# Kernel optimization log

Measured on AMD Instinct MI355X. Metric: run time of the kernel, lower is better.

Reference implementation:

```python
import jax, jax.numpy as jnp
import numpy as np

BETA = 1.0
POWER_ITERS = 9
EPS = 1e-12  # F.normalize default eps


def _normalize(v):
    # L2 normalize over dim=1 of [B, N, 1], matching F.normalize(x, dim=1)
    n = jnp.linalg.norm(v, axis=1, keepdims=True)
    return v / jnp.maximum(n, EPS)


def _dominant_eigenvalue(A, x):
    # A: [B, N, N], x: [B, N, 1]
    for _ in range(POWER_ITERS):
        x = _normalize(jnp.matmul(A, x))
    Ax = jnp.matmul(A, x)[..., 0]              # [B, N]
    num = jnp.sum(Ax * x[..., 0], axis=1)      # x^T A x
    den = jnp.sum(x[..., 0] ** 2, axis=1)      # ||x||^2 (== 1 after normalize)
    return num / den, x


def setup_inputs() -> dict:
    key = jax.random.key(0)
    k1, k2 = jax.random.split(key)
    B, C, H, W = 256, 2048, 7, 7
    x = jax.random.normal(k1, (B, C, H, W), dtype=jnp.float32)
    x0 = _normalize(jax.random.normal(k2, (B, H * W, 1), dtype=jnp.float32))
    return {"x": x, "x0": x0}


def reference(x, x0):
    B, C, H, W = x.shape
    N = H * W
    Wm = x.reshape(B, C, N)
    # ATA = W^T W : [B, N, N]
    ATA = jnp.einsum('bcn,bcm->bnm', Wm, Wm)
    # first power iteration: largest eigenvalue; x0 is a no_grad constant
    largest, x1 = _dominant_eigenvalue(ATA, jax.lax.stop_gradient(x0))
    I = jnp.eye(N, dtype=ATA.dtype)
    shifted = ATA - largest[:, None, None] * I
    # second power iteration warm-started from detached x1 (torch stores last_x detached)
    tmp, _ = _dominant_eigenvalue(shifted, jax.lax.stop_gradient(x1))
    smallest = tmp + largest
    penalty = BETA * (largest / smallest - 1.0) ** 2
    return jnp.sum(penalty) / B
```

## Files before the change

### kernel.cpp

```cpp
#include <hip/hip_runtime.h>
#include <hip/hip_bf16.h>
#include <stdint.h>


#define BATCH 256
#define CDIM  2048
#define NDIM  49
#define QK    512
#define NQ    4
#define CHUNK 64
#define NCHUNK (QK / CHUNK)
#define CHUNK_FLOATS (CHUNK * NDIM)
#define CHUNK_F4 (CHUNK_FLOATS / 4)
#define CPAD (CHUNK_FLOATS + 16)
#define PSIZE (NDIM * NDIM)
#define ASTRIDE 53

typedef __bf16 bf16x8 __attribute__((ext_vector_type(8)));
typedef float  f32x16 __attribute__((ext_vector_type(16)));

__device__ inline void async_load16(const float* g, float* l) {
  __builtin_amdgcn_global_load_lds(
      (const __attribute__((address_space(1))) void*)g,
      (__attribute__((address_space(3))) void*)l,
      16 , 0 , 0 );
}

__global__ __launch_bounds__(256, 4) void gram_kernel(
    const float* __restrict__ x, float* __restrict__ partial,
    float* __restrict__ out) {
  __shared__ float raw[2][CPAD];

  const int tid  = threadIdx.x;
  const int bidx = blockIdx.x;
  const int batch = bidx >> 2;
  const int q     = bidx & 3;
  const int lane = tid & 63;
  const int wv   = tid >> 6;
  const int ln   = lane & 31;
  const int hf   = lane >> 5;
  const int qm   = wv >> 1, qn = wv & 1;
  const int m = qm * 32 + ln;
  const int n = qn * 32 + ln;

  if (bidx == 0 && tid == 0) out[0] = 0.f;

  const float* gbase = x + (size_t)batch * (CDIM * NDIM)
                         + (size_t)q * (QK * NDIM);

  f32x16 c1, c2, c3;
#pragma unroll
  for (int i = 0; i < 16; ++i) { c1[i] = 0.f; c2[i] = 0.f; c3[i] = 0.f; }

#pragma unroll
  for (int i = 0; i < (CHUNK_F4 + 255) / 256; ++i) {
    int slot = i * 256 + tid;
    if (slot < CHUNK_F4) async_load16(gbase + slot * 4, &raw[0][slot * 4]);
  }

  for (int ch = 0; ch < NCHUNK; ++ch) {
    __syncthreads();
    const int cur = ch & 1;
    if (ch + 1 < NCHUNK) {
      const float* gch = gbase + (ch + 1) * CHUNK_FLOATS;
      float* dst = raw[cur ^ 1];
#pragma unroll
      for (int i = 0; i < (CHUNK_F4 + 255) / 256; ++i) {
        int slot = i * 256 + tid;
        if (slot < CHUNK_F4) async_load16(gch + slot * 4, &dst[slot * 4]);
      }
    }

    const float* buf = raw[cur];
#pragma unroll
    for (int s = 0; s < CHUNK / 16; ++s) {
      const int kk = s * 16 + hf * 8;
      const float* pa = &buf[kk * NDIM + m];
      const float* pb = &buf[kk * NDIM + n];
      bf16x8 ah, al, bh, bl;
#pragma unroll
      for (int j = 0; j < 8; ++j) {
        float av = pa[j * NDIM];
        __bf16 h = (__bf16)av;
        ah[j] = h;
        al[j] = (__bf16)(av - (float)h);
        float bv = pb[j * NDIM];
        __bf16 hb = (__bf16)bv;
        bh[j] = hb;
        bl[j] = (__bf16)(bv - (float)hb);
      }
      c1 = __builtin_amdgcn_mfma_f32_32x32x16_bf16(ah, bh, c1, 0, 0, 0);
      c2 = __builtin_amdgcn_mfma_f32_32x32x16_bf16(ah, bl, c2, 0, 0, 0);
      c3 = __builtin_amdgcn_mfma_f32_32x32x16_bf16(al, bh, c3, 0, 0, 0);
    }
  }

  float* outp = partial + (size_t)bidx * PSIZE;
#pragma unroll
  for (int r = 0; r < 16; ++r) {
    int row = (r & 3) + 8 * (r >> 2) + 4 * hf;
    int mm = qm * 32 + row;
    if (mm < NDIM && n < NDIM)
      outp[mm * NDIM + n] = c1[r] + c2[r] + c3[r];
  }
}

__global__ __launch_bounds__(64) void eigen_kernel(
    const float* __restrict__ partial, const float* __restrict__ x0,
    float* __restrict__ out) {
  __shared__ float A[NDIM * ASTRIDE];
  __shared__ float xv[64];

  const int b = blockIdx.x;
  const int t = threadIdx.x;
  const float* p0 = partial + (size_t)(NQ * b) * PSIZE;

  for (int idx = t; idx < NDIM * NDIM; idx += 64) {
    int r = idx / NDIM;
    int c = idx - r * NDIM;
    float v = 0.f;
#pragma unroll
    for (int qq = 0; qq < NQ; ++qq) v += p0[qq * PSIZE + idx];
    A[r * ASTRIDE + c] = v;
  }
  if (t < NDIM) xv[t] = x0[b * NDIM + t];
  __syncthreads();

  auto rayleigh_power = [&](float shift) -> float {
    for (int it = 0; it < 9; ++it) {
      float y = 0.f;
      if (t < NDIM) {
        const float* Ar = &A[t * ASTRIDE];
#pragma unroll 7
        for (int k = 0; k < NDIM; ++k) y = fmaf(Ar[k], xv[k], y);
        y -= shift * xv[t];
      }
      float s = y * y;
#pragma unroll
      for (int o = 32; o; o >>= 1) s += __shfl_xor(s, o, 64);
      float nrm = fmaxf(sqrtf(s), 1e-12f);
      __syncthreads();
      if (t < NDIM) xv[t] = y / nrm;
      __syncthreads();
    }
    float yy = 0.f;
    if (t < NDIM) {
      const float* Ar = &A[t * ASTRIDE];
#pragma unroll 7
      for (int k = 0; k < NDIM; ++k) yy = fmaf(Ar[k], xv[k], yy);
      yy -= shift * xv[t];
    }
    float num = (t < NDIM) ? yy * xv[t] : 0.f;
    float den = (t < NDIM) ? xv[t] * xv[t] : 0.f;
#pragma unroll
    for (int o = 32; o; o >>= 1) {
      num += __shfl_xor(num, o, 64);
      den += __shfl_xor(den, o, 64);
    }
    return num / den;
  };

  float largest = rayleigh_power(0.f);
  float tmp = rayleigh_power(largest);
  float smallest = tmp + largest;

  if (t == 0) {
    float r = largest / smallest - 1.f;
    atomicAdd(out, r * r * (1.0f / (float)BATCH));
  }
}

extern "C" void kernel_launch(void* const* d_in, const int* in_sizes, int n_in,
                              void* d_out, int out_size, void* d_ws,
                              size_t ws_size, hipStream_t stream) {
  const float* x  = (const float*)d_in[0];
  const float* x0 = (const float*)d_in[1];
  float* out = (float*)d_out;
  float* partial = (float*)d_ws;

  gram_kernel<<<1024, 256, 0, stream>>>(x, partial, out);
  eigen_kernel<<<BATCH, 64, 0, stream>>>(partial, x0, out);
}
```

Baseline: 177.7 us.

## Fuse Gram and eigen kernels with last-block reduction and symmetric split-bf16 MFMA

Merges the Gram-matrix kernel and the eigenvalue kernel into one launch. The last of the four quarter-blocks per batch, found through an atomic counter, sums the partials and runs the power iterations. The split-bf16 product drops one of three MFMAs by using symmetry: the al*bh term is taken from the transpose of ah*bl, staged through LDS. Loads switch from async global-to-LDS copies of raw fp32 to register prefetch with the bf16 hi/lo conversion done once before storing to LDS. This saves a launch and removes redundant conversions and MFMAs, but adds a memset, atomics and fences, and the eigen phase now runs inside a 256-thread block in which only a few threads do work.

New measurement: 355.9 us. 2x slower.

```diff
diff --git a/kernel.cpp b/kernel.cpp
--- a/kernel.cpp
+++ b/kernel.cpp
@@ -7,130 +7,145 @@
 #define CDIM  2048
 #define NDIM  49
 #define QK    512
-#define NQ    4
 #define CHUNK 64
 #define NCHUNK (QK / CHUNK)
-#define CHUNK_FLOATS (CHUNK * NDIM)
-#define CHUNK_F4 (CHUNK_FLOATS / 4)
-#define CPAD (CHUNK_FLOATS + 16)
+#define KP    72
+#define TILE_ELEMS (64 * KP)
 #define PSIZE (NDIM * NDIM)
-#define ASTRIDE 53
+#define ESTR  65
+#define ASTR  53
+#define CNT_OFF (1024 * PSIZE)
 
 typedef __bf16 bf16x8 __attribute__((ext_vector_type(8)));
 typedef float  f32x16 __attribute__((ext_vector_type(16)));
 
-__device__ inline void async_load16(const float* g, float* l) {
-  __builtin_amdgcn_global_load_lds(
-      (const __attribute__((address_space(1))) void*)g,
-      (__attribute__((address_space(3))) void*)l,
-      16 , 0 , 0 );
-}
-
-__global__ __launch_bounds__(256, 4) void gram_kernel(
-    const float* __restrict__ x, float* __restrict__ partial,
+__global__ __launch_bounds__(256, 4) void ofpenalty_fused(
+    const float* __restrict__ x, const float* __restrict__ x0,
+    float* __restrict__ partial, unsigned int* __restrict__ cnt,
+    float* __restrict__ acc, unsigned int* __restrict__ done,
     float* __restrict__ out) {
-  __shared__ float raw[2][CPAD];
-
-  const int tid  = threadIdx.x;
-  const int bidx = blockIdx.x;
+  __shared__ __align__(16) char smem[4 * TILE_ELEMS * 2];
+  __shared__ int flag;
+  __bf16* tile = (__bf16*)smem;
+  float* Ebuf  = (float*)smem;
+  float* Aeig  = (float*)smem;
+  float* xv    = (float*)(smem + 10400);
+
+  const int tid   = threadIdx.x;
+  const int bidx  = blockIdx.x;
   const int batch = bidx >> 2;
   const int q     = bidx & 3;
-  const int lane = tid & 63;
-  const int wv   = tid >> 6;
-  const int ln   = lane & 31;
-  const int hf   = lane >> 5;
-  const int qm   = wv >> 1, qn = wv & 1;
-  const int m = qm * 32 + ln;
+  const int w     = tid >> 6;
+  const int lane  = tid & 63;
+  const int ln    = lane & 31;
+  const int hf    = lane >> 5;
+  const int qm = w >> 1, qn = w & 1;
+  const int rowA = qm * 32 + ln;
+  const int rowB = qn * 32 + ln;
+
+  const float* gbase = x + ((size_t)batch * CDIM + (size_t)q * QK) * NDIM;
+
+  f32x16 c1, cE;
+#pragma unroll
+  for (int i = 0; i < 16; ++i) { c1[i] = 0.f; cE[i] = 0.f; }
+
+  float L[2][8];
+
+  if (lane < NDIM) {
+#pragma unroll
+    for (int kk = 0; kk < 2; ++kk) {
+      const int kg = w + kk * 4;
+#pragma unroll
+      for (int j = 0; j < 8; ++j)
+        L[kk][j] = gbase[(size_t)(kg * 8 + j) * NDIM + lane];
+    }
+  }
+
+  for (int ch = 0; ch < NCHUNK; ++ch) {
+    const int buf = ch & 1;
+    if (lane < NDIM) {
+#pragma unroll
+      for (int kk = 0; kk < 2; ++kk) {
+        const int kg = w + kk * 4;
+        bf16x8 h8, l8;
+#pragma unroll
+        for (int j = 0; j < 8; ++j) {
+          float v = L[kk][j];
+          __bf16 h = (__bf16)v;
+          h8[j] = h;
+          l8[j] = (__bf16)(v - (float)h);
+        }
+        *(bf16x8*)(tile + (buf * 2 + 0) * TILE_ELEMS + lane * KP + kg * 8) = h8;
+        *(bf16x8*)(tile + (buf * 2 + 1) * TILE_ELEMS + lane * KP + kg * 8) = l8;
+      }
+    }
+    __syncthreads();
+    if (ch + 1 < NCHUNK && lane < NDIM) {
+      const float* cb = gbase + (size_t)((ch + 1) * CHUNK) * NDIM + lane;
+#pragma unroll
+      for (int kk = 0; kk < 2; ++kk) {
+        const int kg = w + kk * 4;
+#pragma unroll
+        for (int j = 0; j < 8; ++j)
+          L[kk][j] = cb[(size_t)(kg * 8 + j) * NDIM];
+      }
+    }
+    const __bf16* th = tile + (buf * 2 + 0) * TILE_ELEMS;
+    const __bf16* tl = tile + (buf * 2 + 1) * TILE_ELEMS;
+#pragma unroll
+    for (int s = 0; s < 4; ++s) {
+      const int g = s * 2 + hf;
+      bf16x8 ah = *(const bf16x8*)(th + rowA * KP + g * 8);
+      bf16x8 bh = *(const bf16x8*)(th + rowB * KP + g * 8);
+      bf16x8 bl = *(const bf16x8*)(tl + rowB * KP + g * 8);
+      c1 = __builtin_amdgcn_mfma_f32_32x32x16_bf16(ah, bh, c1, 0, 0, 0);
+      cE = __builtin_amdgcn_mfma_f32_32x32x16_bf16(ah, bl, cE, 0, 0, 0);
+    }
+  }
+
+  __syncthreads();
+#pragma unroll
+  for (int r = 0; r < 16; ++r) {
+    const int mm = qm * 32 + (r & 3) + 8 * (r >> 2) + 4 * hf;
+    Ebuf[mm * ESTR + (qn * 32 + ln)] = cE[r];
+  }
+  __syncthreads();
+  float* outp = partial + (size_t)bidx * PSIZE;
   const int n = qn * 32 + ln;
-
-  if (bidx == 0 && tid == 0) out[0] = 0.f;
-
-  const float* gbase = x + (size_t)batch * (CDIM * NDIM)
-                         + (size_t)q * (QK * NDIM);
-
-  f32x16 c1, c2, c3;
-#pragma unroll
-  for (int i = 0; i < 16; ++i) { c1[i] = 0.f; c2[i] = 0.f; c3[i] = 0.f; }
-
-#pragma unroll
-  for (int i = 0; i < (CHUNK_F4 + 255) / 256; ++i) {
-    int slot = i * 256 + tid;
-    if (slot < CHUNK_F4) async_load16(gbase + slot * 4, &raw[0][slot * 4]);
-  }
-
-  for (int ch = 0; ch < NCHUNK; ++ch) {
-    __syncthreads();
-    const int cur = ch & 1;
-    if (ch + 1 < NCHUNK) {
-      const float* gch = gbase + (ch + 1) * CHUNK_FLOATS;
-      float* dst = raw[cur ^ 1];
-#pragma unroll
-      for (int i = 0; i < (CHUNK_F4 + 255) / 256; ++i) {
-        int slot = i * 256 + tid;
-        if (slot < CHUNK_F4) async_load16(gch + slot * 4, &dst[slot * 4]);
-      }
-    }
-
-    const float* buf = raw[cur];
-#pragma unroll
-    for (int s = 0; s < CHUNK / 16; ++s) {
-      const int kk = s * 16 + hf * 8;
-      const float* pa = &buf[kk * NDIM + m];
-      const float* pb = &buf[kk * NDIM + n];
-      bf16x8 ah, al, bh, bl;
-#pragma unroll
-      for (int j = 0; j < 8; ++j) {
-        float av = pa[j * NDIM];
-        __bf16 h = (__bf16)av;
-        ah[j] = h;
-        al[j] = (__bf16)(av - (float)h);
-        float bv = pb[j * NDIM];
-        __bf16 hb = (__bf16)bv;
-        bh[j] = hb;
-        bl[j] = (__bf16)(bv - (float)hb);
-      }
-      c1 = __builtin_amdgcn_mfma_f32_32x32x16_bf16(ah, bh, c1, 0, 0, 0);
-      c2 = __builtin_amdgcn_mfma_f32_32x32x16_bf16(ah, bl, c2, 0, 0, 0);
-      c3 = __builtin_amdgcn_mfma_f32_32x32x16_bf16(al, bh, c3, 0, 0, 0);
-    }
-  }
-
-  float* outp = partial + (size_t)bidx * PSIZE;
 #pragma unroll
   for (int r = 0; r < 16; ++r) {
-    int row = (r & 3) + 8 * (r >> 2) + 4 * hf;
-    int mm = qm * 32 + row;
+    const int mm = qm * 32 + (r & 3) + 8 * (r >> 2) + 4 * hf;
     if (mm < NDIM && n < NDIM)
-      outp[mm * NDIM + n] = c1[r] + c2[r] + c3[r];
-  }
-}
-
-__global__ __launch_bounds__(64) void eigen_kernel(
-    const float* __restrict__ partial, const float* __restrict__ x0,
-    float* __restrict__ out) {
-  __shared__ float A[NDIM * ASTRIDE];
-  __shared__ float xv[64];
-
-  const int b = blockIdx.x;
-  const int t = threadIdx.x;
-  const float* p0 = partial + (size_t)(NQ * b) * PSIZE;
-
-  for (int idx = t; idx < NDIM * NDIM; idx += 64) {
-    int r = idx / NDIM;
-    int c = idx - r * NDIM;
+      outp[mm * NDIM + n] = c1[r] + cE[r] + Ebuf[n * ESTR + mm];
+  }
+
+  __threadfence();
+  __syncthreads();
+  if (tid == 0) {
+    unsigned int old = atomicAdd(&cnt[batch], 1u);
+    flag = (old == 3u) ? 1 : 0;
+  }
+  __syncthreads();
+  if (!flag) return;
+  __threadfence();
+
+  const float* p0 = partial + (size_t)(batch * 4) * PSIZE;
+  for (int idx = tid; idx < PSIZE; idx += 256) {
+    int r = idx / NDIM, c = idx - r * NDIM;
     float v = 0.f;
 #pragma unroll
-    for (int qq = 0; qq < NQ; ++qq) v += p0[qq * PSIZE + idx];
-    A[r * ASTRIDE + c] = v;
-  }
-  if (t < NDIM) xv[t] = x0[b * NDIM + t];
-  __syncthreads();
-
+    for (int qq = 0; qq < 4; ++qq) v += p0[qq * PSIZE + idx];
+    Aeig[r * ASTR + c] = v;
+  }
+  if (tid < NDIM) xv[tid] = x0[batch * NDIM + tid];
+  __syncthreads();
+
+  const int t = tid;
   auto rayleigh_power = [&](float shift) -> float {
     for (int it = 0; it < 9; ++it) {
       float y = 0.f;
       if (t < NDIM) {
-        const float* Ar = &A[t * ASTRIDE];
+        const float* Ar = &Aeig[t * ASTR];
 #pragma unroll 7
         for (int k = 0; k < NDIM; ++k) y = fmaf(Ar[k], xv[k], y);
         y -= shift * xv[t];
@@ -145,7 +160,7 @@
     }
     float yy = 0.f;
     if (t < NDIM) {
-      const float* Ar = &A[t * ASTRIDE];
+      const float* Ar = &Aeig[t * ASTR];
 #pragma unroll 7
       for (int k = 0; k < NDIM; ++k) yy = fmaf(Ar[k], xv[k], yy);
       yy -= shift * xv[t];
@@ -166,7 +181,13 @@
 
   if (t == 0) {
     float r = largest / smallest - 1.f;
-    atomicAdd(out, r * r * (1.0f / (float)BATCH));
+    atomicAdd(acc, r * r * (1.0f / (float)BATCH));
+    __threadfence();
+    unsigned int od = atomicAdd(done, 1u);
+    if (od == BATCH - 1) {
+      __threadfence();
+      out[0] = atomicAdd(acc, 0.0f);
+    }
   }
 }
 
@@ -177,7 +198,10 @@
   const float* x0 = (const float*)d_in[1];
   float* out = (float*)d_out;
   float* partial = (float*)d_ws;
-
-  gram_kernel<<<1024, 256, 0, stream>>>(x, partial, out);
-  eigen_kernel<<<BATCH, 64, 0, stream>>>(partial, x0, out);
+  unsigned int* cnt  = (unsigned int*)(partial + CNT_OFF);
+  float*        acc  = (float*)(cnt + 256);
+  unsigned int* done = (unsigned int*)(cnt + 257);
+
+  hipMemsetAsync((void*)cnt, 0, 258 * sizeof(unsigned int), stream);
+  ofpenalty_fused<<<1024, 256, 0, stream>>>(x, x0, partial, cnt, acc, done, out);
 }
```

## Pre-split bf16 hi/lo tiles in LDS and derive cross term via transpose

Applied to the files above, without the earlier changes.

Each chunk is now converted once into bf16 high and low tiles in shared memory, so waves no longer redo the fp32-to-bf16 split for their own A and B fragments. Because the Gram matrix is symmetric, the al*bh cross term is taken as the transpose of the ah*bl accumulator, written through a padded LDS buffer, which drops one of the three MFMAs per step. The cost is an extra barrier per chunk, more LDS use, and an epilogue transpose through shared memory.

New measurement: 179.3 us. No clear change (+0.9%).

```diff
diff --git a/kernel.cpp b/kernel.cpp
--- a/kernel.cpp
+++ b/kernel.cpp
@@ -7,14 +7,17 @@
 #define CDIM  2048
 #define NDIM  49
 #define QK    512
-#define NQ    4
 #define CHUNK 64
 #define NCHUNK (QK / CHUNK)
-#define CHUNK_FLOATS (CHUNK * NDIM)
-#define CHUNK_F4 (CHUNK_FLOATS / 4)
-#define CPAD (CHUNK_FLOATS + 16)
+#define CH_FLOATS (CHUNK * NDIM)
+#define CH_SLOTS  (CH_FLOATS / 4)
+#define TN    56
+#define NSLICE (8 * TN)
+#define TILE_BYTES (8 * TN * 8 * 2)
+#define RAW_BYTES (2 * CH_FLOATS * 4)
 #define PSIZE (NDIM * NDIM)
-#define ASTRIDE 53
+#define ESTR  65
+#define ASTR  53
 
 typedef __bf16 bf16x8 __attribute__((ext_vector_type(8)));
 typedef float  f32x16 __attribute__((ext_vector_type(16)));
@@ -29,99 +32,132 @@
 __global__ __launch_bounds__(256, 4) void gram_kernel(
     const float* __restrict__ x, float* __restrict__ partial,
     float* __restrict__ out) {
-  __shared__ float raw[2][CPAD];
-
-  const int tid  = threadIdx.x;
-  const int bidx = blockIdx.x;
+  __shared__ __align__(16) char smem[RAW_BYTES + 2 * TILE_BYTES];
+  float*  raw0 = (float*)smem;
+  float*  raw1 = (float*)(smem + CH_FLOATS * 4);
+  __bf16* tH   = (__bf16*)(smem + RAW_BYTES);
+  __bf16* tL   = (__bf16*)(smem + RAW_BYTES + TILE_BYTES);
+  float*  Ebuf = (float*)smem;
+
+  const int tid   = threadIdx.x;
+  const int bidx  = blockIdx.x;
   const int batch = bidx >> 2;
   const int q     = bidx & 3;
-  const int lane = tid & 63;
-  const int wv   = tid >> 6;
-  const int ln   = lane & 31;
-  const int hf   = lane >> 5;
-  const int qm   = wv >> 1, qn = wv & 1;
-  const int m = qm * 32 + ln;
-  const int n = qn * 32 + ln;
+  const int w     = tid >> 6;
+  const int lane  = tid & 63;
+  const int ln    = lane & 31;
+  const int hf    = lane >> 5;
+  const int qm = w >> 1, qn = w & 1;
+  const int rowA = min(qm * 32 + ln, TN - 1);
+  const int rowB = min(qn * 32 + ln, TN - 1);
+  const int nOut = qn * 32 + ln;
 
   if (bidx == 0 && tid == 0) out[0] = 0.f;
 
-  const float* gbase = x + (size_t)batch * (CDIM * NDIM)
-                         + (size_t)q * (QK * NDIM);
-
-  f32x16 c1, c2, c3;
-#pragma unroll
-  for (int i = 0; i < 16; ++i) { c1[i] = 0.f; c2[i] = 0.f; c3[i] = 0.f; }
-
-#pragma unroll
-  for (int i = 0; i < (CHUNK_F4 + 255) / 256; ++i) {
+  const float* gbase = x + ((size_t)batch * CDIM + (size_t)q * QK) * NDIM;
+
+  f32x16 c1, cE;
+#pragma unroll
+  for (int i = 0; i < 16; ++i) { c1[i] = 0.f; cE[i] = 0.f; }
+
+  const int s1ok = (tid < NSLICE - 256);
+  const int n0 = tid % TN,         g0 = tid / TN;
+  const int n1 = (256 + tid) % TN, g1 = (256 + tid) / TN;
+
+#pragma unroll
+  for (int i = 0; i < 4; ++i) {
     int slot = i * 256 + tid;
-    if (slot < CHUNK_F4) async_load16(gbase + slot * 4, &raw[0][slot * 4]);
+    if (slot < CH_SLOTS) async_load16(gbase + slot * 4, raw0 + slot * 4);
   }
 
   for (int ch = 0; ch < NCHUNK; ++ch) {
+    float* cur = (ch & 1) ? raw1 : raw0;
+    float* nxt = (ch & 1) ? raw0 : raw1;
     __syncthreads();
-    const int cur = ch & 1;
+
     if (ch + 1 < NCHUNK) {
-      const float* gch = gbase + (ch + 1) * CHUNK_FLOATS;
-      float* dst = raw[cur ^ 1];
-#pragma unroll
-      for (int i = 0; i < (CHUNK_F4 + 255) / 256; ++i) {
+      const float* gch = gbase + (size_t)(ch + 1) * CH_FLOATS;
+#pragma unroll
+      for (int i = 0; i < 4; ++i) {
         int slot = i * 256 + tid;
-        if (slot < CHUNK_F4) async_load16(gch + slot * 4, &dst[slot * 4]);
-      }
-    }
-
-    const float* buf = raw[cur];
-#pragma unroll
-    for (int s = 0; s < CHUNK / 16; ++s) {
-      const int kk = s * 16 + hf * 8;
-      const float* pa = &buf[kk * NDIM + m];
-      const float* pb = &buf[kk * NDIM + n];
-      bf16x8 ah, al, bh, bl;
+        if (slot < CH_SLOTS) async_load16(gch + slot * 4, nxt + slot * 4);
+      }
+    }
+
+    if (n0 < NDIM) {
+      const float* rp = cur + g0 * 8 * NDIM + n0;
+      bf16x8 h8, l8;
 #pragma unroll
       for (int j = 0; j < 8; ++j) {
-        float av = pa[j * NDIM];
-        __bf16 h = (__bf16)av;
-        ah[j] = h;
-        al[j] = (__bf16)(av - (float)h);
-        float bv = pb[j * NDIM];
-        __bf16 hb = (__bf16)bv;
-        bh[j] = hb;
-        bl[j] = (__bf16)(bv - (float)hb);
-      }
+        float v = rp[j * NDIM];
+        __bf16 h = (__bf16)v;
+        h8[j] = h;
+        l8[j] = (__bf16)(v - (float)h);
+      }
+      *(bf16x8*)(tH + (g0 * TN + n0) * 8) = h8;
+      *(bf16x8*)(tL + (g0 * TN + n0) * 8) = l8;
+    }
+    if (s1ok && n1 < NDIM) {
+      const float* rp = cur + g1 * 8 * NDIM + n1;
+      bf16x8 h8, l8;
+#pragma unroll
+      for (int j = 0; j < 8; ++j) {
+        float v = rp[j * NDIM];
+        __bf16 h = (__bf16)v;
+        h8[j] = h;
+        l8[j] = (__bf16)(v - (float)h);
+      }
+      *(bf16x8*)(tH + (g1 * TN + n1) * 8) = h8;
+      *(bf16x8*)(tL + (g1 * TN + n1) * 8) = l8;
+    }
+    __syncthreads();
+
+#pragma unroll
+    for (int g2 = 0; g2 < 4; ++g2) {
+      const int g = g2 * 2 + hf;
+      bf16x8 ah = *(const bf16x8*)(tH + (g * TN + rowA) * 8);
+      bf16x8 bh;
+      if (qm == qn) bh = ah;
+      else          bh = *(const bf16x8*)(tH + (g * TN + rowB) * 8);
+      bf16x8 bl = *(const bf16x8*)(tL + (g * TN + rowB) * 8);
       c1 = __builtin_amdgcn_mfma_f32_32x32x16_bf16(ah, bh, c1, 0, 0, 0);
-      c2 = __builtin_amdgcn_mfma_f32_32x32x16_bf16(ah, bl, c2, 0, 0, 0);
-      c3 = __builtin_amdgcn_mfma_f32_32x32x16_bf16(al, bh, c3, 0, 0, 0);
-    }
-  }
-
+      cE = __builtin_amdgcn_mfma_f32_32x32x16_bf16(ah, bl, cE, 0, 0, 0);
+    }
+  }
+
+  __syncthreads();
+#pragma unroll
+  for (int r = 0; r < 16; ++r) {
+    const int mm = qm * 32 + (r & 3) + 8 * (r >> 2) + 4 * hf;
+    Ebuf[mm * ESTR + nOut] = cE[r];
+  }
+  __syncthreads();
   float* outp = partial + (size_t)bidx * PSIZE;
 #pragma unroll
   for (int r = 0; r < 16; ++r) {
-    int row = (r & 3) + 8 * (r >> 2) + 4 * hf;
-    int mm = qm * 32 + row;
-    if (mm < NDIM && n < NDIM)
-      outp[mm * NDIM + n] = c1[r] + c2[r] + c3[r];
+    const int mm = qm * 32 + (r & 3) + 8 * (r >> 2) + 4 * hf;
+    if (mm < NDIM && nOut < NDIM)
+      outp[mm * NDIM + nOut] = c1[r] + cE[r] + Ebuf[nOut * ESTR + mm];
   }
 }
 
 __global__ __launch_bounds__(64) void eigen_kernel(
     const float* __restrict__ partial, const float* __restrict__ x0,
     float* __restrict__ out) {
-  __shared__ float A[NDIM * ASTRIDE];
+  __shared__ float A[NDIM * ASTR];
   __shared__ float xv[64];
 
   const int b = blockIdx.x;
   const int t = threadIdx.x;
-  const float* p0 = partial + (size_t)(NQ * b) * PSIZE;
+  const float* p0 = partial + (size_t)(4 * b) * PSIZE;
 
   for (int idx = t; idx < NDIM * NDIM; idx += 64) {
     int r = idx / NDIM;
     int c = idx - r * NDIM;
     float v = 0.f;
 #pragma unroll
-    for (int qq = 0; qq < NQ; ++qq) v += p0[qq * PSIZE + idx];
-    A[r * ASTRIDE + c] = v;
+    for (int qq = 0; qq < 4; ++qq) v += p0[qq * PSIZE + idx];
+    A[r * ASTR + c] = v;
   }
   if (t < NDIM) xv[t] = x0[b * NDIM + t];
   __syncthreads();
@@ -130,7 +166,7 @@
     for (int it = 0; it < 9; ++it) {
       float y = 0.f;
       if (t < NDIM) {
-        const float* Ar = &A[t * ASTRIDE];
+        const float* Ar = &A[t * ASTR];
 #pragma unroll 7
         for (int k = 0; k < NDIM; ++k) y = fmaf(Ar[k], xv[k], y);
         y -= shift * xv[t];
@@ -145,7 +181,7 @@
     }
     float yy = 0.f;
     if (t < NDIM) {
-      const float* Ar = &A[t * ASTRIDE];
+      const float* Ar = &A[t * ASTR];
 #pragma unroll 7
       for (int k = 0; k < NDIM; ++k) yy = fmaf(Ar[k], xv[k], yy);
       yy -= shift * xv[t];
```
